# Optimization experiments

Measured on AMD Instinct MI355X. Metric: run time of the kernel, lower is better.

Reference implementation:

```python
import jax, jax.numpy as jnp
import numpy as np

C = 256; GC = 32; G = C // GC; K = 3; S = 1; NEW = 2; PAD = (K - 1) // 2
IN1 = C * K * 2 + C * K * K // 32          # 1608
OUT1 = G * NEW * NEW * K * K // 4          # 72
OUT2 = G * NEW * NEW * K * K               # 288
B = 8; H = 56; W = 56


def setup_inputs():
    key = jax.random.key(0)
    k0, k1, k2 = jax.random.split(key, 3)
    inputs = jax.random.normal(k0, (B, C, H, W), jnp.float32)
    W1 = jax.random.normal(k1, (OUT1, IN1), jnp.float32) * np.float32(1.0 / np.sqrt(IN1))
    b1 = jnp.zeros((OUT1,), jnp.float32)
    W2 = jax.random.normal(k2, (OUT2, OUT1), jnp.float32) * np.float32(1.0 / np.sqrt(OUT1))
    b2 = jnp.zeros((OUT2,), jnp.float32)
    return {"inputs": inputs, "W1": W1, "b1": b1, "W2": W2, "b2": b2}


def _unfold(x, h, w):
    # torch.nn.Unfold(K, 1, PAD, S): patches of shape (B, C, K, K, h, w)
    xp = jnp.pad(x, ((0, 0), (0, 0), (PAD, PAD), (PAD, PAD)))
    cols = [xp[:, :, di:di + (h - 1) * S + 1:S, dj:dj + (w - 1) * S + 1:S]
            for di in range(K) for dj in range(K)]  # fixed K*K=9 slices
    return jnp.stack(cols, axis=2).reshape(x.shape[0], x.shape[1], K, K, h, w)


def reference(inputs, W1, b1, W2, b2):
    b, c, Hh, Ww = inputs.shape
    h = (Hh + 2 * PAD - K) // S + 1
    w = (Ww + 2 * PAD - K) // S + 1
    # (B, G, GC, K, K, h, w)
    x = _unfold(inputs, h, w).reshape(b, G, GC, K, K, h, w)
    # three max-pooled descriptors over different axes
    x1 = x.reshape(b, G, -1, GC // 32, K, K, h, w).max(axis=2).reshape(b, -1, h, w)  # (B, C*K*K//32, h, w)
    x2 = x.max(axis=3).reshape(b, -1, h, w)  # (B, C*K, h, w)
    x3 = x.max(axis=4).reshape(b, -1, h, w)  # (B, C*K, h, w)
    feat = jnp.concatenate([x1, x2, x3], axis=1)  # (B, IN1, h, w)
    # two biased 1x1 convs (ConvModule with no norm/act)
    y = jnp.einsum('bchw,oc->bohw', feat, W1) + b1[None, :, None, None]
    y = jnp.einsum('bchw,oc->bohw', y, W2) + b2[None, :, None, None]
    # softmax over the K*K kernel-window dim
    wgt = jax.nn.softmax(y.reshape(b, G, K * K, NEW * NEW, h, w), axis=2)
    # softmax-weighted local aggregation: sum over kernel window
    agg = jnp.einsum('bgckhw,bgknhw->bgcnhw', x.reshape(b, G, GC, K * K, h, w), wgt)
    # fold with non-overlapping (NEW, NEW) blocks == block upsampling reshape
    return agg.reshape(b, C, NEW, NEW, h, w).transpose(0, 1, 4, 2, 5, 3).reshape(b, C, h * NEW, w * NEW)
```

## Files before the change

kernel.cpp:

```cpp
#include <hip/hip_runtime.h>

#define CC   256
#define HH   56
#define WWID 56
#define KIN1 1608
#define KP1  1632
#define NO1  72
#define NO2  288
#define PPB  14
#define H2   112
#define W2D  112

typedef unsigned short u16;
typedef unsigned int   u32;
typedef __attribute__((ext_vector_type(8))) short v8s;
typedef __attribute__((ext_vector_type(4))) float v4f;

#define W1BF_ELEMS (80 * KP1)
#define W2BF_OFF_B 262144

#define LDS_TOTAL 40192
#define OFF_A 0
#define OFF_B 24832
#define OFF_C 33280
#define OFF_D 36608

__device__ __forceinline__ u16 f2b(float x) {
  u32 u = __float_as_uint(x);
  u = (u + 0x7FFFu + ((u >> 16) & 1u)) >> 16;
  return (u16)u;
}

__global__ void kConvW(const float* __restrict__ W1, const float* __restrict__ W2,
                       u16* __restrict__ w1bf, u16* __restrict__ w2bf) {
  int idx = blockIdx.x * 256 + threadIdx.x;
  if (idx < W1BF_ELEMS) {
    int m = idx / KP1, k = idx - m * KP1;
    float v = 0.f;
    if (m < NO1) {
      int orig = -1;
      if (k < 768)                 orig = 72 + (k & 255) * 3 + (k >> 8);
      else if (k < 1536)           orig = 840 + (k & 255) * 3 + ((k - 768) >> 8);
      else if ((k - 1536) < NO1)   orig = k - 1536;
      if (orig >= 0) v = W1[m * KIN1 + orig];
    }
    w1bf[idx] = f2b(v);
  } else {
    int i2 = idx - W1BF_ELEMS;
    if (i2 < NO2 * 96) {
      int m = i2 / 96, k = i2 - m * 96;
      w2bf[i2] = (k < NO1) ? f2b(W2[m * NO1 + k]) : (u16)0;
    }
  }
}

__global__ __launch_bounds__(256, 4)
void kFused(const float* __restrict__ in, const u16* __restrict__ w1bf,
            const float* __restrict__ b1, const u16* __restrict__ w2bf,
            const float* __restrict__ b2, float* __restrict__ out) {
  __shared__ __align__(16) char lds[LDS_TOTAL];
  u16*   rowmaxT = (u16*)(lds + OFF_A);
  u16*   colmaxT = (u16*)(lds + OFF_B);
  u16*   x1T     = (u16*)(lds + OFF_C);
  float* gmax_s  = (float*)(lds + OFF_D);
  float* partA   = (float*)(lds + OFF_A);
  float* y2L     = (float*)(lds + OFF_A);
  float* tile    = (float*)(lds + OFF_B);

  const int t  = threadIdx.x;
  {
  }
  const int L  = blockIdx.x + 4 * (blockIdx.y + 56 * blockIdx.z);
  const int jq = L >> 3;
  const int jt = jq & 3, i = jq >> 2, b = L & 7;
  const int c  = t;
  const int g  = c >> 5;
  const int gc = c & 31;
  const int w  = t >> 6, lane = t & 63;
  const int ml = lane & 15, quad = lane >> 4;

  {
    u32* xu = (u32*)x1T;
    if (t < 132) {
#pragma unroll
      for (int rp2 = 0; rp2 < 2; ++rp2) {
        int idx = 2 * t + rp2;
        if (idx < 192) { int row = idx / 12; xu[row * 52 + 36 + (idx - row * 12)] = 0u; }
        else { int e = idx - 192; xu[(14 + e / 36) * 52 + (e % 36)] = 0u; }
      }
    }
  }

  const float* rowbase0 = in + ((size_t)b * CC + c) * (HH * WWID);
  u32 win_p[3][8];
  float colmax[16];
#pragma unroll
  for (int k = 0; k < 16; ++k) colmax[k] = -3.0e38f;

#pragma unroll
  for (int r = 0; r < 3; ++r) {
    const int row = i - 1 + r;
    float sc[16];
    if (row < 0 || row >= HH) {
#pragma unroll
      for (int k = 0; k < 16; ++k) sc[k] = 0.f;
    } else {
      const float* rp = rowbase0 + row * WWID;
      float l[20];
      if (jt == 0) {
        const float4 a0 = *(const float4*)(rp), a1 = *(const float4*)(rp + 4),
                     a2 = *(const float4*)(rp + 8), a3 = *(const float4*)(rp + 12);
        l[0]=a0.x;l[1]=a0.y;l[2]=a0.z;l[3]=a0.w; l[4]=a1.x;l[5]=a1.y;l[6]=a1.z;l[7]=a1.w;
        l[8]=a2.x;l[9]=a2.y;l[10]=a2.z;l[11]=a2.w; l[12]=a3.x;l[13]=a3.y;l[14]=a3.z;l[15]=a3.w;
        sc[0] = 0.f;
#pragma unroll
        for (int k = 1; k < 16; ++k) sc[k] = l[k - 1];
      } else if (jt == 3) {
        const float* q = rp + 40;
        const float4 a0 = *(const float4*)(q), a1 = *(const float4*)(q + 4),
                     a2 = *(const float4*)(q + 8), a3 = *(const float4*)(q + 12);
        l[0]=a0.x;l[1]=a0.y;l[2]=a0.z;l[3]=a0.w; l[4]=a1.x;l[5]=a1.y;l[6]=a1.z;l[7]=a1.w;
        l[8]=a2.x;l[9]=a2.y;l[10]=a2.z;l[11]=a2.w; l[12]=a3.x;l[13]=a3.y;l[14]=a3.z;l[15]=a3.w;
#pragma unroll
        for (int k = 0; k < 15; ++k) sc[k] = l[k + 1];
        sc[15] = 0.f;
      } else {
        const float* q = rp + ((jt == 1) ? 12 : 24);
        const float4 a0 = *(const float4*)(q), a1 = *(const float4*)(q + 4),
                     a2 = *(const float4*)(q + 8), a3 = *(const float4*)(q + 12),
                     a4 = *(const float4*)(q + 16);
        l[0]=a0.x;l[1]=a0.y;l[2]=a0.z;l[3]=a0.w; l[4]=a1.x;l[5]=a1.y;l[6]=a1.z;l[7]=a1.w;
        l[8]=a2.x;l[9]=a2.y;l[10]=a2.z;l[11]=a2.w; l[12]=a3.x;l[13]=a3.y;l[14]=a3.z;l[15]=a3.w;
        l[16]=a4.x;l[17]=a4.y;l[18]=a4.z;l[19]=a4.w;
        if (jt == 1) {
#pragma unroll
          for (int k = 0; k < 16; ++k) sc[k] = l[k + 1];
        } else {
#pragma unroll
          for (int k = 0; k < 16; ++k) sc[k] = l[k + 3];
        }
      }
    }
#pragma unroll
    for (int k = 0; k < 16; ++k) colmax[k] = fmaxf(colmax[k], sc[k]);
#pragma unroll
    for (int n = 0; n < 14; ++n)
      rowmaxT[n * 776 + r * 256 + c] = f2b(fmaxf(fmaxf(sc[n], sc[n + 1]), sc[n + 2]));
#pragma unroll
    for (int col = 0; col < 16; ++col) {
      float m = sc[col];
      m = fmaxf(m, __shfl_xor(m, 1));
      m = fmaxf(m, __shfl_xor(m, 2));
      m = fmaxf(m, __shfl_xor(m, 4));
      m = fmaxf(m, __shfl_xor(m, 8));
      m = fmaxf(m, __shfl_xor(m, 16));
      if (gc == col) gmax_s[g * 48 + r * 16 + col] = m;
    }
#pragma unroll
    for (int k = 0; k < 8; ++k)
      win_p[r][k] = (u32)f2b(sc[2 * k]) | ((u32)f2b(sc[2 * k + 1]) << 16);
  }
#pragma unroll
  for (int col = 0; col < 16; ++col)
    colmaxT[col * 264 + c] = f2b(colmax[col]);
  asm volatile("s_waitcnt lgkmcnt(0)" ::: "memory");
#pragma unroll
  for (int rep = 0; rep < 4; ++rep) {
    int idx = gc + 32 * rep;
    if (idx < 126) {
      int n = idx / 9, r9 = idx - n * 9, ki = r9 / 3, kj = r9 - ki * 3;
      x1T[n * 104 + g * 9 + r9] = f2b(gmax_s[g * 48 + ki * 16 + n + kj]);
    }
  }
  __syncthreads();

  v4f acc[5];
#pragma unroll
  for (int mt = 0; mt < 5; ++mt) acc[mt] = (v4f){0.f, 0.f, 0.f, 0.f};
  const int ks0 = w * 13, ks1 = (w == 3) ? 51 : ks0 + 13;

  auto loadB = [&](int ks) -> v8s {
    if (ks < 24) {
      int kj = ks >> 3, c0 = (ks & 7) * 32;
      return *(v8s*)&colmaxT[(ml + kj) * 264 + c0 + quad * 8];
    } else if (ks < 48) {
      return *(v8s*)&rowmaxT[ml * 776 + (ks - 24) * 32 + quad * 8];
    } else {
      return *(v8s*)&x1T[ml * 104 + (ks - 48) * 32 + quad * 8];
    }
  };

  {
    v8s bf_c = loadB(ks0);
    v8s af_c[5];
    {
      const int k0 = ks0 * 32 + quad * 8;
#pragma unroll
      for (int mt = 0; mt < 5; ++mt)
        af_c[mt] = *(const v8s*)&w1bf[(mt * 16 + ml) * KP1 + k0];
    }
    for (int ks = ks0; ks < ks1; ++ks) {
      v8s bf_n, af_n[5];
      if (ks + 1 < ks1) {
        bf_n = loadB(ks + 1);
        const int k0n = (ks + 1) * 32 + quad * 8;
#pragma unroll
        for (int mt = 0; mt < 5; ++mt)
          af_n[mt] = *(const v8s*)&w1bf[(mt * 16 + ml) * KP1 + k0n];
      }
#pragma unroll
      for (int mt = 0; mt < 5; ++mt)
        acc[mt] = __builtin_amdgcn_mfma_f32_16x16x32_bf16(af_c[mt], bf_c, acc[mt], 0, 0, 0);
      if (ks + 1 < ks1) {
        bf_c = bf_n;
#pragma unroll
        for (int mt = 0; mt < 5; ++mt) af_c[mt] = af_n[mt];
      }
    }
  }
  __syncthreads();

#pragma unroll
  for (int mt = 0; mt < 5; ++mt)
    *(v4f*)&partA[((w * 5 + mt) * 16 + ml) * 16 + quad * 4] = acc[mt];
  __syncthreads();

  u16* y1b = x1T;
#pragma unroll
  for (int it = 0; it < 4; ++it) {
    int e = t + it * 256;
    if (e < NO1 * PPB) {
      int m = e / PPB, n = e - m * PPB;
      float s = b1[m];
#pragma unroll
      for (int ww = 0; ww < 4; ++ww)
        s += partA[((ww * 5 + (m >> 4)) * 16 + n) * 16 + (m & 15)];
      y1b[n * 104 + m] = f2b(s);
    }
  }
  __syncthreads();

  {
    v8s bfr[3];
#pragma unroll
    for (int ks = 0; ks < 3; ++ks)
      bfr[ks] = *(v8s*)&y1b[ml * 104 + ks * 32 + quad * 8];
    const int mt0 = (w < 2) ? 5 * w : 10 + 4 * (w - 2);
    const int mtn = (w < 2) ? 5 : 4;
    for (int mi = 0; mi < mtn; ++mi) {
      const int mt = mt0 + mi;
      v4f a2 = (v4f){0.f, 0.f, 0.f, 0.f};
#pragma unroll
      for (int ks = 0; ks < 3; ++ks) {
        v8s af = *(const v8s*)&w2bf[(mt * 16 + ml) * 96 + ks * 32 + quad * 8];
        a2 = __builtin_amdgcn_mfma_f32_16x16x32_bf16(af, bfr[ks], a2, 0, 0, 0);
      }
      const int o0 = mt * 16 + quad * 4;
      const float4 bv = *(const float4*)(b2 + o0);
      a2[0] += bv.x; a2[1] += bv.y; a2[2] += bv.z; a2[3] += bv.w;
      *(v4f*)&y2L[ml * 296 + o0] = a2;
    }
  }
  __syncthreads();

#pragma unroll
  for (int it = 0; it < 2; ++it) {
    int s2 = t + it * 256;
    if (s2 < 448) {
      int gg = s2 / 56, rem = s2 - gg * 56, nn = rem / PPB, n = rem - nn * PPB;
      float* bp = &y2L[n * 296 + gg * 36 + nn];
      float v9[9], m = -1e30f;
#pragma unroll
      for (int k = 0; k < 9; ++k) { v9[k] = bp[k * 4]; m = fmaxf(m, v9[k]); }
      float sum = 0.f;
#pragma unroll
      for (int k = 0; k < 9; ++k) { v9[k] = __expf(v9[k] - m); sum += v9[k]; }
      float inv = 1.f / sum;
#pragma unroll
      for (int k = 0; k < 9; ++k) bp[k * 4] = v9[k] * inv;
    }
  }
  __syncthreads();

  float a0s[14], a1s[14], a2s[14], a3s[14];
#pragma unroll
  for (int n = 0; n < 14; ++n) {
    const v4f* wp = (const v4f*)&y2L[n * 296 + g * 36];
    float a0 = 0.f, a1 = 0.f, a2v = 0.f, a3 = 0.f;
#pragma unroll
    for (int r = 0; r < 3; ++r) {
      float x0, x1, x2v;
      if ((n & 1) == 0) {
        u32 ua = win_p[r][n >> 1], ub = win_p[r][(n >> 1) + 1];
        x0  = __uint_as_float(ua << 16);
        x1  = __uint_as_float(ua & 0xffff0000u);
        x2v = __uint_as_float(ub << 16);
      } else {
        u32 ua = win_p[r][n >> 1], ub = win_p[r][(n >> 1) + 1];
        x0  = __uint_as_float(ua & 0xffff0000u);
        x1  = __uint_as_float(ub << 16);
        x2v = __uint_as_float(ub & 0xffff0000u);
      }
#pragma unroll
      for (int kj = 0; kj < 3; ++kj) {
        v4f wv = wp[r * 3 + kj];
        float x = (kj == 0) ? x0 : (kj == 1) ? x1 : x2v;
        a0  = fmaf(x, wv[0], a0);
        a1  = fmaf(x, wv[1], a1);
        a2v = fmaf(x, wv[2], a2v);
        a3  = fmaf(x, wv[3], a3);
      }
    }
    a0s[n] = a0; a1s[n] = a1; a2s[n] = a2v; a3s[n] = a3;
  }

  const int cl = c & 63;
  for (int ch = 0; ch < 4; ++ch) {
    if ((c >> 6) == ch) {
#pragma unroll
      for (int n = 0; n < 14; ++n) {
        float2 lo2; lo2.x = a0s[n]; lo2.y = a1s[n];
        float2 hi2; hi2.x = a2s[n]; hi2.y = a3s[n];
        *(float2*)&tile[cl * 60 + 2 * n] = lo2;
        *(float2*)&tile[cl * 60 + 28 + 2 * n] = hi2;
      }
    }
    __syncthreads();
#pragma unroll
    for (int it = 0; it < 4; ++it) {
      int f = t + it * 256;
      if (f < 896) {
        int rr = f / 7, xi = f - rr * 7;
        int cg = ch * 64 + (rr >> 1), di = rr & 1;
        v4f val = *(v4f*)&tile[(rr >> 1) * 60 + di * 28 + xi * 4];
        *(v4f*)&out[((size_t)(b * CC + cg) * H2 + (size_t)(2 * i + di)) * W2D
                    + 28 * jt + xi * 4] = val;
      }
    }
    __syncthreads();
  }
}

extern "C" void kernel_launch(void* const* d_in, const int* in_sizes, int n_in,
                              void* d_out, int out_size, void* d_ws, size_t ws_size,
                              hipStream_t stream) {
  const float* in = (const float*)d_in[0];
  const float* W1 = (const float*)d_in[1];
  const float* b1 = (const float*)d_in[2];
  const float* W2 = (const float*)d_in[3];
  const float* b2 = (const float*)d_in[4];
  float* out = (float*)d_out;

  u16* w1bf = (u16*)d_ws;
  u16* w2bf = (u16*)((char*)d_ws + W2BF_OFF_B);

  const int B = in_sizes[0] / (CC * HH * WWID);

  kConvW<<<dim3((W1BF_ELEMS + NO2 * 96 + 255) / 256), 256, 0, stream>>>(W1, W2, w1bf, w2bf);
  dim3 grid(WWID / PPB, HH, B);
  kFused<<<grid, 256, 0, stream>>>(in, w1bf, b1, w2bf, b2, out);
}
```

Before: 205.8 us.

## Shrink LDS with XOR swizzle, direct x1T writes, and raise occupancy

Replaces the padded LDS row strides with unpadded strides plus an XOR swizzle, which keeps bank-conflict avoidance while cutting shared memory from about 40KB to 32KB. The gmax_s staging buffer is removed: the pooled group max is written directly into every x1T slot that uses it, and the output tile now aliases region A. Launch bounds go from 4 to 5 blocks per CU to exploit the smaller LDS footprint. An extra barrier is added before the tile reuse, and the tighter register budget risks spills.

```diff
diff --git a/kernel.cpp b/kernel.cpp
--- a/kernel.cpp
+++ b/kernel.cpp
@@ -19,11 +19,12 @@
 #define W1BF_ELEMS (80 * KP1)
 #define W2BF_OFF_B 262144
 
-#define LDS_TOTAL 40192
+#define LDS_TOTAL 32768
 #define OFF_A 0
-#define OFF_B 24832
-#define OFF_C 33280
-#define OFF_D 36608
+#define OFF_B 21504
+#define OFF_C 29696
+
+#define SWZ(row) (((row) & 7) << 3)
 
 __device__ __forceinline__ u16 f2b(float x) {
   u32 u = __float_as_uint(x);
@@ -54,7 +55,7 @@
   }
 }
 
-__global__ __launch_bounds__(256, 4)
+__global__ __launch_bounds__(256, 5)
 void kFused(const float* __restrict__ in, const u16* __restrict__ w1bf,
             const float* __restrict__ b1, const u16* __restrict__ w2bf,
             const float* __restrict__ b2, float* __restrict__ out) {
@@ -62,14 +63,11 @@
   u16*   rowmaxT = (u16*)(lds + OFF_A);
   u16*   colmaxT = (u16*)(lds + OFF_B);
   u16*   x1T     = (u16*)(lds + OFF_C);
-  float* gmax_s  = (float*)(lds + OFF_D);
   float* partA   = (float*)(lds + OFF_A);
   float* y2L     = (float*)(lds + OFF_A);
-  float* tile    = (float*)(lds + OFF_B);
+  float* tile    = (float*)(lds + OFF_A);
 
   const int t  = threadIdx.x;
-  {
-  }
   const int L  = blockIdx.x + 4 * (blockIdx.y + 56 * blockIdx.z);
   const int jq = L >> 3;
   const int jt = jq & 3, i = jq >> 2, b = L & 7;
@@ -85,8 +83,13 @@
 #pragma unroll
       for (int rp2 = 0; rp2 < 2; ++rp2) {
         int idx = 2 * t + rp2;
-        if (idx < 192) { int row = idx / 12; xu[row * 52 + 36 + (idx - row * 12)] = 0u; }
-        else { int e = idx - 192; xu[(14 + e / 36) * 52 + (e % 36)] = 0u; }
+        if (idx < 192) {
+          int row = idx / 12;
+          xu[(row * 48 + 36 + (idx - row * 12)) ^ ((row & 7) << 2)] = 0u;
+        } else {
+          int e = idx - 192, row = 14 + e / 36;
+          xu[(row * 48 + (e % 36)) ^ ((row & 7) << 2)] = 0u;
+        }
       }
     }
   }
@@ -145,7 +148,8 @@
     for (int k = 0; k < 16; ++k) colmax[k] = fmaxf(colmax[k], sc[k]);
 #pragma unroll
     for (int n = 0; n < 14; ++n)
-      rowmaxT[n * 776 + r * 256 + c] = f2b(fmaxf(fmaxf(sc[n], sc[n + 1]), sc[n + 2]));
+      rowmaxT[(n * 768 + r * 256 + c) ^ SWZ(n)] =
+          f2b(fmaxf(fmaxf(sc[n], sc[n + 1]), sc[n + 2]));
 #pragma unroll
     for (int col = 0; col < 16; ++col) {
       float m = sc[col];
@@ -154,7 +158,15 @@
       m = fmaxf(m, __shfl_xor(m, 4));
       m = fmaxf(m, __shfl_xor(m, 8));
       m = fmaxf(m, __shfl_xor(m, 16));
-      if (gc == col) gmax_s[g * 48 + r * 16 + col] = m;
+      if (gc == col) {
+        u16 mv = f2b(m);
+#pragma unroll
+        for (int kj = 0; kj < 3; ++kj) {
+          const int n = col - kj;
+          if (n >= 0 && n < 14)
+            x1T[(n * 96 + g * 9 + r * 3 + kj) ^ SWZ(n)] = mv;
+        }
+      }
     }
 #pragma unroll
     for (int k = 0; k < 8; ++k)
@@ -162,16 +174,7 @@
   }
 #pragma unroll
   for (int col = 0; col < 16; ++col)
-    colmaxT[col * 264 + c] = f2b(colmax[col]);
-  asm volatile("s_waitcnt lgkmcnt(0)" ::: "memory");
-#pragma unroll
-  for (int rep = 0; rep < 4; ++rep) {
-    int idx = gc + 32 * rep;
-    if (idx < 126) {
-      int n = idx / 9, r9 = idx - n * 9, ki = r9 / 3, kj = r9 - ki * 3;
-      x1T[n * 104 + g * 9 + r9] = f2b(gmax_s[g * 48 + ki * 16 + n + kj]);
-    }
-  }
+    colmaxT[(col * 256 + c) ^ SWZ(col)] = f2b(colmax[col]);
   __syncthreads();
 
   v4f acc[5];
@@ -181,12 +184,12 @@
 
   auto loadB = [&](int ks) -> v8s {
     if (ks < 24) {
-      int kj = ks >> 3, c0 = (ks & 7) * 32;
-      return *(v8s*)&colmaxT[(ml + kj) * 264 + c0 + quad * 8];
+      int kj = ks >> 3, c0 = (ks & 7) * 32, rowi = ml + kj;
+      return *(v8s*)&colmaxT[(rowi * 256 + c0 + quad * 8) ^ SWZ(rowi)];
     } else if (ks < 48) {
-      return *(v8s*)&rowmaxT[ml * 776 + (ks - 24) * 32 + quad * 8];
+      return *(v8s*)&rowmaxT[(ml * 768 + (ks - 24) * 32 + quad * 8) ^ SWZ(ml)];
     } else {
-      return *(v8s*)&x1T[ml * 104 + (ks - 48) * 32 + quad * 8];
+      return *(v8s*)&x1T[(ml * 96 + (ks - 48) * 32 + quad * 8) ^ SWZ(ml)];
     }
   };
 
@@ -235,7 +238,7 @@
 #pragma unroll
       for (int ww = 0; ww < 4; ++ww)
         s += partA[((ww * 5 + (m >> 4)) * 16 + n) * 16 + (m & 15)];
-      y1b[n * 104 + m] = f2b(s);
+      y1b[(n * 96 + m) ^ SWZ(n)] = f2b(s);
     }
   }
   __syncthreads();
@@ -244,7 +247,7 @@
     v8s bfr[3];
 #pragma unroll
     for (int ks = 0; ks < 3; ++ks)
-      bfr[ks] = *(v8s*)&y1b[ml * 104 + ks * 32 + quad * 8];
+      bfr[ks] = *(v8s*)&y1b[(ml * 96 + ks * 32 + quad * 8) ^ SWZ(ml)];
     const int mt0 = (w < 2) ? 5 * w : 10 + 4 * (w - 2);
     const int mtn = (w < 2) ? 5 : 4;
     for (int mi = 0; mi < mtn; ++mi) {
@@ -313,6 +316,7 @@
     }
     a0s[n] = a0; a1s[n] = a1; a2s[n] = a2v; a3s[n] = a3;
   }
+  __syncthreads();
 
   const int cl = c & 63;
   for (int ch = 0; ch < 4; ++ch) {
```

Measured after the change: 273.9 us. 1.33x slower.
